# Kernel optimization log

Hardware: AMD Instinct MI355X
Metric: run time of the kernel (lower is better)

The kernel has to match this reference:

```python
import jax, jax.numpy as jnp
import numpy as np

SCORE_THR = 0.05
IOU_THR = 0.5
STD = np.array([0.1, 0.1, 0.2, 0.2], dtype=np.float32)


def _regress_and_clip(reg_pred, anchors, h, w):
    # reg_pred [B,4,A], anchors [A,4] (x1,y1,x2,y2) -> boxes [B,A,4]
    std = jnp.asarray(STD)
    widths = anchors[:, 2] - anchors[:, 0]
    heights = anchors[:, 3] - anchors[:, 1]
    cx = anchors[:, 0] + 0.5 * widths
    cy = anchors[:, 1] + 0.5 * heights
    reg = reg_pred * std[None, :, None]
    dx, dy, dw, dh = reg[:, 0], reg[:, 1], reg[:, 2], reg[:, 3]  # each [B,A]
    pred_cx = cx + dx * widths
    pred_cy = cy + dy * heights
    pred_w = jnp.exp(dw) * widths
    pred_h = jnp.exp(dh) * heights
    x1 = jnp.maximum(pred_cx - 0.5 * pred_w, 0.0)
    y1 = pred_cy - 0.5 * pred_h
    x2 = pred_cx + 0.5 * pred_w
    y2 = pred_cy + 0.5 * pred_h
    # clip_anchors
    x1 = jnp.maximum(x1, 0.0)
    y1 = jnp.maximum(y1, 0.0)
    x2 = jnp.minimum(x2, jnp.float32(w))
    y2 = jnp.minimum(y2, jnp.float32(h))
    return jnp.stack([x1, y1, x2, y2], axis=-1)  # [B,A,4] (= permuted boxes_pred)


def _iou_one_vs_all(box, boxes):
    ix1 = jnp.maximum(box[0], boxes[:, 0])
    iy1 = jnp.maximum(box[1], boxes[:, 1])
    ix2 = jnp.minimum(box[2], boxes[:, 2])
    iy2 = jnp.minimum(box[3], boxes[:, 3])
    inter = jnp.maximum(ix2 - ix1, 0.0) * jnp.maximum(iy2 - iy1, 0.0)
    a0 = (box[2] - box[0]) * (box[3] - box[1])
    a1 = (boxes[:, 2] - boxes[:, 0]) * (boxes[:, 3] - boxes[:, 1])
    return inter / jnp.maximum(a0 + a1 - inter, 1e-9)


def _nms_keep(boxes, scores):
    # Greedy NMS (torchvision semantics): returns bool keep mask over all anchors.
    valid = scores > SCORE_THR
    order = jnp.argsort(jnp.where(valid, -scores, jnp.inf))  # desc by score, invalid last
    b = boxes[order]
    keep0 = valid[order]
    n = boxes.shape[0]
    idx = jnp.arange(n)
    def body(i, keep):
        iou = _iou_one_vs_all(b[i], b)
        sup = keep[i] & (iou > IOU_THR) & (idx > i)
        return keep & (~sup)
    keep_sorted = jax.lax.fori_loop(0, n, body, keep0)
    return jnp.zeros(n, dtype=bool).at[order].set(keep_sorted)


def _keep_mask(boxes, cls_pred):
    # boxes [B,A,4], cls_pred [B,C,A] -> keep [B,C,A]
    per_class = jax.vmap(_nms_keep, in_axes=(None, 0))
    return jax.vmap(per_class, in_axes=(0, 0))(boxes, cls_pred)


def setup_inputs() -> dict:
    key = jax.random.key(0)
    k1, k2, k3, k4 = jax.random.split(key, 4)
    B, C, A, H, W = 2, 80, 1024, 2048, 2048
    image = jax.random.normal(k1, (B, 3, H, W), dtype=jnp.float32)
    cls_pred = jax.random.uniform(k2, (B, C, A), dtype=jnp.float32)  # sigmoid-like scores
    reg_pred = jax.random.normal(k3, (B, 4, A), dtype=jnp.float32)
    kc, ks = jax.random.split(k4)
    cxy = jax.random.uniform(kc, (A, 2), minval=0.0, maxval=float(W), dtype=jnp.float32)
    wh = jax.random.uniform(ks, (A, 2), minval=16.0, maxval=256.0, dtype=jnp.float32)
    anchors = jnp.concatenate([cxy - 0.5 * wh, cxy + 0.5 * wh], axis=1)  # [A,4] x1y1x2y2
    return {"image": image, "cls_pred": cls_pred, "reg_pred": reg_pred, "anchors": anchors}


def reference(image, cls_pred, reg_pred, anchors):
    B, _, H, W = image.shape
    boxes = _regress_and_clip(reg_pred, anchors, H, W)      # [B,A,4]
    keep = _keep_mask(boxes, cls_pred)                      # [B,C,A] bool
    scores_out = jnp.where(keep, cls_pred, 0.0)             # [B,C,A]
    boxes_out = jnp.where(keep[..., None], boxes[:, None, :, :], 0.0)  # [B,C,A,4]
    # Fixed-shape packing of the module's ragged [scores, cls, boxes] output:
    # per (batch, class, anchor): (score, x1, y1, x2, y2), zeros where suppressed.
    return jnp.concatenate([scores_out[..., None], boxes_out], axis=-1)  # [B,C,A,5]
```

## Files before the change

kernel.cpp:

```cpp
#include <hip/hip_runtime.h>
#include <stdint.h>

#define BATCH 2
#define NCLS 80
#define NP (BATCH * NCLS)
#define NA 1024
#define NWORD 16
#define NWBLK 64
#define IMG_W 2048.0f
#define IMG_H 2048.0f

__device__ __forceinline__ unsigned enc_f32(float f) {
  unsigned u = __float_as_uint(f);
  return (u & 0x80000000u) ? ~u : (u | 0x80000000u);
}

__device__ __forceinline__ unsigned long long shflx64(unsigned long long v, int m) {
  int lo = __shfl_xor((int)(unsigned)v, m, 64);
  int hi = __shfl_xor((int)(unsigned)(v >> 32), m, 64);
  return ((unsigned long long)(unsigned)hi << 32) | (unsigned)lo;
}

__device__ __forceinline__ void cas64(unsigned long long& x, unsigned long long& y, bool up) {
  if ((x > y) == up) { unsigned long long t = x; x = y; y = t; }
}

__global__ __launch_bounds__(256) void prep_kernel(
    const float* __restrict__ cls_pred,
    const float* __restrict__ reg_pred,
    const float* __restrict__ anchors,
    unsigned long long* __restrict__ skeyG,
    float4* __restrict__ sboxG,
    int* __restrict__ nvalidG,
    unsigned long long* __restrict__ W)
{
#pragma clang fp contract(off)
  const int tid = threadIdx.x;
  __shared__ __align__(16) unsigned char smem[24832];

  if (blockIdx.x < NP) {
    const int bc = blockIdx.x;
    const int b  = bc / NCLS;
    float4*             obox = (float4*)(smem);
    unsigned long long* skey = (unsigned long long*)(smem + 16384);
    int*                cntS = (int*)(smem + 24576);

    if (tid == 0) *cntS = 0;
    __syncthreads();

    const float* regb = reg_pred + (size_t)b * 4 * NA;
    const float* scb  = cls_pred + (size_t)bc * NA;

    float4 s4 = ((const float4*)scb)[tid];
    float4 x4 = ((const float4*)(regb + 0 * NA))[tid];
    float4 y4 = ((const float4*)(regb + 1 * NA))[tid];
    float4 w4 = ((const float4*)(regb + 2 * NA))[tid];
    float4 h4 = ((const float4*)(regb + 3 * NA))[tid];
    float ss[4]  = {s4.x, s4.y, s4.z, s4.w};
    float dxs[4] = {x4.x, x4.y, x4.z, x4.w};
    float dys[4] = {y4.x, y4.y, y4.z, y4.w};
    float dws[4] = {w4.x, w4.y, w4.z, w4.w};
    float dhs[4] = {h4.x, h4.y, h4.z, h4.w};

    unsigned long long r[4];
    int localcnt = 0;
#pragma unroll
    for (int m = 0; m < 4; ++m) {
      const int a = tid * 4 + m;
      float4 an = ((const float4*)anchors)[a];
      float w  = an.z - an.x;
      float h  = an.w - an.y;
      float cx = an.x + 0.5f * w;
      float cy = an.y + 0.5f * h;
      float dx = dxs[m] * 0.1f;
      float dy = dys[m] * 0.1f;
      float dw = dws[m] * 0.2f;
      float dh = dhs[m] * 0.2f;
      float pcx = cx + dx * w;
      float pcy = cy + dy * h;
      float pw  = expf(dw) * w;
      float ph  = expf(dh) * h;
      float x1 = fmaxf(pcx - 0.5f * pw, 0.0f);
      float y1 = pcy - 0.5f * ph;
      x1 = fmaxf(x1, 0.0f);
      y1 = fmaxf(y1, 0.0f);
      float x2 = fminf(pcx + 0.5f * pw, IMG_W);
      float y2 = fminf(pcy + 0.5f * ph, IMG_H);
      obox[a] = make_float4(x1, y1, x2, y2);

      float s    = ss[m];
      bool valid = (s > 0.05f);
      localcnt  += valid ? 1 : 0;
      float key  = valid ? -s : __int_as_float(0x7f800000);
      r[m] = ((unsigned long long)enc_f32(key) << 32) | (unsigned)a;
    }
    atomicAdd(cntS, localcnt);

#pragma unroll
    for (int kk = 1; kk <= 10; ++kk) {
      const int k = 1 << kk;
#pragma unroll
      for (int jj = kk - 1; jj >= 0; --jj) {
        const int j = 1 << jj;
        if (j >= 256) {
          __syncthreads();
#pragma unroll
          for (int m = 0; m < 4; ++m) skey[tid * 4 + m] = r[m];
          __syncthreads();
#pragma unroll
          for (int m = 0; m < 4; ++m) {
            const int e = tid * 4 + m;
            unsigned long long o = skey[e ^ j];
            const bool up = ((e & k) == 0);
            const bool lo = ((e & j) == 0);
            unsigned long long mn = (r[m] < o) ? r[m] : o;
            unsigned long long mx = (r[m] < o) ? o : r[m];
            r[m] = (lo == up) ? mn : mx;
          }
        } else if (j >= 4) {
          const int d = j >> 2;
          const bool lo = ((tid & d) == 0);
#pragma unroll
          for (int m = 0; m < 4; ++m) {
            const int e = tid * 4 + m;
            const bool up = ((e & k) == 0);
            unsigned long long o = shflx64(r[m], d);
            unsigned long long mn = (r[m] < o) ? r[m] : o;
            unsigned long long mx = (r[m] < o) ? o : r[m];
            r[m] = (lo == up) ? mn : mx;
          }
        } else if (j == 2) {
          const bool up = (((tid * 4) & k) == 0);
          cas64(r[0], r[2], up);
          cas64(r[1], r[3], up);
        } else {
          const bool up01 = (((tid * 4 + 0) & k) == 0);
          const bool up23 = (((tid * 4 + 2) & k) == 0);
          cas64(r[0], r[1], up01);
          cas64(r[2], r[3], up23);
        }
      }
    }

    unsigned long long* pk = skeyG + (size_t)bc * NA;
    float4* pb = sboxG + (size_t)bc * NA;
#pragma unroll
    for (int m = 0; m < 4; ++m) {
      unsigned long long kv = r[m];
      pk[tid * 4 + m] = kv;
      pb[tid * 4 + m] = obox[(int)(unsigned)kv];
    }
    if (tid == 0) nvalidG[bc] = *cntS;

  } else {
    const int wb   = blockIdx.x - NP;
    const int b    = wb >> 5;
    const int sub  = wb & 31;
    const int rblk = sub >> 1;
    const int qh   = sub & 1;
    const int lane = tid & 63;
    const int wq   = tid >> 6;

    float4* sb = (float4*)(smem);

    const float* regb = reg_pred + (size_t)b * 4 * NA;
    for (int a = tid; a < NA; a += 256) {
      float4 an = ((const float4*)anchors)[a];
      float w  = an.z - an.x;
      float h  = an.w - an.y;
      float cx = an.x + 0.5f * w;
      float cy = an.y + 0.5f * h;
      float dx = regb[0 * NA + a] * 0.1f;
      float dy = regb[1 * NA + a] * 0.1f;
      float dw = regb[2 * NA + a] * 0.2f;
      float dh = regb[3 * NA + a] * 0.2f;
      float pcx = cx + dx * w;
      float pcy = cy + dy * h;
      float pw  = expf(dw) * w;
      float ph  = expf(dh) * h;
      float x1 = fmaxf(pcx - 0.5f * pw, 0.0f);
      float y1 = pcy - 0.5f * ph;
      x1 = fmaxf(x1, 0.0f);
      y1 = fmaxf(y1, 0.0f);
      float x2 = fminf(pcx + 0.5f * pw, IMG_W);
      float y2 = fminf(pcy + 0.5f * ph, IMG_H);
      sb[a] = make_float4(x1, y1, x2, y2);
    }
    __syncthreads();

    const int r = rblk * 64 + lane;
    float4 br = sb[r];
    float  ar = (br.z - br.x) * (br.w - br.y);
    unsigned long long* wrow = W + ((size_t)b * NA + r) * NWORD;

#pragma unroll
    for (int k2 = 0; k2 < 2; ++k2) {
      const int kw = qh * 8 + wq * 2 + k2;
      const int jbase = kw * 64;
      unsigned long long bits = 0ull;
#pragma unroll 8
      for (int jj = 0; jj < 64; ++jj) {
        float4 bj = sb[jbase + jj];
        float  aj = (bj.z - bj.x) * (bj.w - bj.y);
        float ix1 = fmaxf(br.x, bj.x);
        float iy1 = fmaxf(br.y, bj.y);
        float ix2 = fminf(br.z, bj.z);
        float iy2 = fminf(br.w, bj.w);
        float inter = fmaxf(ix2 - ix1, 0.0f) * fmaxf(iy2 - iy1, 0.0f);
        float un = fmaxf((ar + aj) - inter, 1e-9f);
        bool sup = ((inter + inter) - un) > un * 5.9604644775390625e-8f;
        bits |= sup ? (1ull << jj) : 0ull;
      }
      wrow[kw] = bits;
    }
  }
}

__global__ __launch_bounds__(128) void scan_kernel(
    const unsigned long long* __restrict__ skeyG,
    const float4* __restrict__ sboxG,
    const unsigned long long* __restrict__ W,
    const int* __restrict__ nvalidG,
    float* __restrict__ out)
{
  const int p    = blockIdx.x;
  const int b    = p / NCLS;
  const int tid  = threadIdx.x;
  const int lane = tid & 63;
  const int wid  = tid >> 6;

  __shared__ unsigned long long rowsL[2][64 * 17];
  __shared__ unsigned long long diagL[2][64];
  __shared__ int oL[NA];
  __shared__ unsigned long long KorigL[NWORD];
  __shared__ unsigned long long keptS[NWORD];
  __shared__ __align__(16) float outAll[NA * 5];

  if (tid < NWORD) { KorigL[tid] = 0ull; keptS[tid] = 0ull; }

  const int nv = nvalidG[p];
  const int nchunk = (nv + 63) >> 6;
  const unsigned long long* pk = skeyG + (size_t)p * NA;
  const unsigned long long* Wb = W + (size_t)b * NA * NWORD;

#pragma unroll
  for (int t = 0; t < 8; ++t) {
    int r = t * 128 + tid;
    oL[r] = (int)(unsigned)pk[r];
  }
  __syncthreads();

  const int rsub = lane >> 4;
  const int wsub = lane & 15;

  if (wid == 1 && nchunk > 0) {
    unsigned long long pre[16];
#pragma unroll
    for (int t = 0; t < 16; ++t) {
      int orow = oL[t * 4 + rsub];
      pre[t] = Wb[(size_t)orow * NWORD + wsub];
    }
#pragma unroll
    for (int t = 0; t < 16; ++t)
      rowsL[0][(t * 4 + rsub) * 17 + wsub] = pre[t];
    int om = oL[lane];
    int wsel = om >> 6, bsel = om & 63;
    unsigned long long d = 0ull;
#pragma unroll 16
    for (int si = 0; si < 64; ++si)
      d |= ((rowsL[0][si * 17 + wsel] >> bsel) & 1ull) << si;
    diagL[0][lane] = d;
  }
  __syncthreads();

  for (int c = 0; c < nchunk; ++c) {
    const int cbuf = c & 1;
    if (wid == 1) {
      if (c + 1 < nchunk) {
        const int nbuf = cbuf ^ 1;
        unsigned long long pre[16];
#pragma unroll
        for (int t = 0; t < 16; ++t) {
          int orow = oL[(c + 1) * 64 + t * 4 + rsub];
          pre[t] = Wb[(size_t)orow * NWORD + wsub];
        }
#pragma unroll
        for (int t = 0; t < 16; ++t)
          rowsL[nbuf][(t * 4 + rsub) * 17 + wsub] = pre[t];
        int om = oL[(c + 1) * 64 + lane];
        int wsel = om >> 6, bsel = om & 63;
        unsigned long long d = 0ull;
#pragma unroll 16
        for (int si = 0; si < 64; ++si)
          d |= ((rowsL[nbuf][si * 17 + wsel] >> bsel) & 1ull) << si;
        diagL[nbuf][lane] = d;
      }
    } else {
      const int sMine = c * 64 + lane;
      const int oMine = oL[sMine];

      unsigned long long pp = 0ull;
      if (c) {
#pragma unroll
        for (int k = 0; k < NWORD; ++k)
          pp |= rowsL[cbuf][lane * 17 + k] & KorigL[k];
      }

      unsigned long long diag = diagL[cbuf][lane] & ((1ull << lane) - 1ull);

      unsigned long long valid = __ballot(sMine < nv);
      unsigned long long S     = __ballot(pp != 0ull);
      unsigned long long K  = 0ull;
      unsigned long long Dd = (~valid) | S;
      for (int round = 0; round < 64; ++round) {
        unsigned long long und = ~Dd;
        if (und == 0ull) break;
        bool me_und  = (und >> lane) & 1ull;
        bool blocked = (diag & (K | und)) != 0ull;
        bool isSupp  = (diag & K) != 0ull;
        unsigned long long kb  = __ballot(me_und && !blocked);
        unsigned long long sbm = __ballot(me_und && isSupp);
        K  |= kb;
        Dd |= kb | sbm;
      }
      if (lane == 0) keptS[c] = K;

      if ((K >> lane) & 1ull)
        atomicOr(&KorigL[oMine >> 6], 1ull << (oMine & 63));
    }
    __syncthreads();
  }

  const float4* pb = sboxG + (size_t)p * NA;
#pragma unroll
  for (int t = 0; t < 8; ++t) {
    int r = t * 128 + tid;
    unsigned long long kv = pk[r];
    float4 bx = pb[r];
    int orig = (int)(unsigned)kv;
    bool kp = (keptS[r >> 6] >> (r & 63)) & 1ull;
    float sc = 0.0f;
    float4 ob = make_float4(0.0f, 0.0f, 0.0f, 0.0f);
    if (kp) {
      sc = -__uint_as_float(~(unsigned)(kv >> 32));
      ob = bx;
    }
    float* oa = outAll + (size_t)orig * 5;
    oa[0] = sc; oa[1] = ob.x; oa[2] = ob.y; oa[3] = ob.z; oa[4] = ob.w;
  }
  __syncthreads();

  float4* og = (float4*)(out + (size_t)p * NA * 5);
  const float4* ol = (const float4*)outAll;
  for (int t4 = tid; t4 < (NA * 5) / 4; t4 += 128) og[t4] = ol[t4];
}

__global__ __launch_bounds__(256) void nms_mono_kernel(
    const float* __restrict__ cls_pred,
    const float* __restrict__ reg_pred,
    const float* __restrict__ anchors,
    float* __restrict__ out)
{
#pragma clang fp contract(off)
  const int bc  = blockIdx.x;
  const int b   = bc / NCLS;
  const int tid = threadIdx.x;
  const int BNT = 256, BPT = 4;

  __shared__ __align__(16) unsigned char smem[49152];
  float4*             obox  = (float4*)(smem);
  float4*             sbox  = (float4*)(smem + 16384);
  unsigned long long* skey  = (unsigned long long*)(smem + 32768);
  float*              sarea = (float*)(smem + 40960);
  int*                keepL = (int*)(smem + 45056);

  const float* regb = reg_pred + (size_t)b * 4 * NA;
  const float* scb  = cls_pred + (size_t)bc * NA;
  for (int a = tid; a < NA; a += BNT) {
    float4 an = ((const float4*)anchors)[a];
    float w  = an.z - an.x;
    float h  = an.w - an.y;
    float cx = an.x + 0.5f * w;
    float cy = an.y + 0.5f * h;
    float dx = regb[0 * NA + a] * 0.1f;
    float dy = regb[1 * NA + a] * 0.1f;
    float dw = regb[2 * NA + a] * 0.2f;
    float dh = regb[3 * NA + a] * 0.2f;
    float pcx = cx + dx * w;
    float pcy = cy + dy * h;
    float pw  = expf(dw) * w;
    float ph  = expf(dh) * h;
    float x1 = fmaxf(fmaxf(pcx - 0.5f * pw, 0.0f), 0.0f);
    float y1 = fmaxf(pcy - 0.5f * ph, 0.0f);
    float x2 = fminf(pcx + 0.5f * pw, IMG_W);
    float y2 = fminf(pcy + 0.5f * ph, IMG_H);
    obox[a] = make_float4(x1, y1, x2, y2);
    float s   = scb[a];
    float key = (s > 0.05f) ? -s : __int_as_float(0x7f800000);
    skey[a] = ((unsigned long long)enc_f32(key) << 32) | (unsigned)a;
  }
  __syncthreads();
  for (int k = 2; k <= NA; k <<= 1) {
    for (int j = k >> 1; j > 0; j >>= 1) {
      for (int m = tid; m < NA; m += BNT) {
        int mx = m ^ j;
        if (mx > m) {
          unsigned long long va = skey[m];
          unsigned long long vb = skey[mx];
          bool up = ((m & k) == 0);
          if ((va > vb) == up) { skey[m] = vb; skey[mx] = va; }
        }
      }
      __syncthreads();
    }
  }
  float4 bj[4]; float aj[4]; int kj[4];
#pragma unroll
  for (int m = 0; m < BPT; ++m) {
    int r = tid + m * BNT;
    unsigned long long kv = skey[r];
    int orig = (int)(unsigned)kv;
    float4 bx = obox[orig];
    sbox[r] = bx;
    float ar = (bx.z - bx.x) * (bx.w - bx.y);
    sarea[r] = ar;
    int kp = ((unsigned)(kv >> 32) != 0xFF800000u) ? 1 : 0;
    keepL[r] = kp;
    bj[m] = bx; aj[m] = ar; kj[m] = kp;
  }
  for (int i = 0; i < NA; ++i) {
    __syncthreads();
    if (keepL[i] == 0) continue;
    float4 bi = sbox[i];
    float  ai = sarea[i];
#pragma unroll
    for (int m = 0; m < BPT; ++m) {
      int j = tid + m * BNT;
      if (j > i && kj[m]) {
        float ix1 = fmaxf(bi.x, bj[m].x);
        float iy1 = fmaxf(bi.y, bj[m].y);
        float ix2 = fminf(bi.z, bj[m].z);
        float iy2 = fminf(bi.w, bj[m].w);
        float inter = fmaxf(ix2 - ix1, 0.0f) * fmaxf(iy2 - iy1, 0.0f);
        float un = fmaxf(ai + aj[m] - inter, 1e-9f);
        if (inter / un > 0.5f) { kj[m] = 0; keepL[j] = 0; }
      }
    }
  }
  __syncthreads();
  float4* outbox = obox;
  float*  outsc  = sarea;
#pragma unroll
  for (int m = 0; m < BPT; ++m) {
    int r = tid + m * BNT;
    unsigned long long kv = skey[r];
    int orig = (int)(unsigned)kv;
    float  sc = 0.0f;
    float4 bx = make_float4(0.0f, 0.0f, 0.0f, 0.0f);
    if (kj[m]) {
      sc = -__uint_as_float(~(unsigned)(kv >> 32));
      bx = sbox[r];
    }
    outsc[orig]  = sc;
    outbox[orig] = bx;
  }
  __syncthreads();
  float* ob = out + (size_t)bc * NA * 5;
  for (int a = tid; a < NA; a += BNT) {
    float4 bx = outbox[a];
    float* o = ob + (size_t)a * 5;
    o[0] = outsc[a]; o[1] = bx.x; o[2] = bx.y; o[3] = bx.z; o[4] = bx.w;
  }
}

extern "C" void kernel_launch(void* const* d_in, const int* in_sizes, int n_in,
                              void* d_out, int out_size, void* d_ws, size_t ws_size,
                              hipStream_t stream) {
  const float* cls = (const float*)d_in[1];
  const float* reg = (const float*)d_in[2];
  const float* anc = (const float*)d_in[3];
  float* out = (float*)d_out;

  const size_t off_key = 0;
  const size_t off_box = off_key + (size_t)NP * NA * 8;
  const size_t off_w   = off_box + (size_t)NP * NA * 16;
  const size_t off_nv  = off_w + (size_t)BATCH * NA * NWORD * 8;
  const size_t need    = off_nv + (size_t)NP * sizeof(int);

  if (ws_size < need) {
    nms_mono_kernel<<<dim3(NP), dim3(256), 0, stream>>>(cls, reg, anc, out);
    return;
  }

  char* ws = (char*)d_ws;
  unsigned long long* skeyG = (unsigned long long*)(ws + off_key);
  float4*             sboxG = (float4*)(ws + off_box);
  unsigned long long* Wm    = (unsigned long long*)(ws + off_w);
  int*                nvG   = (int*)(ws + off_nv);

  prep_kernel<<<dim3(NP + NWBLK), dim3(256), 0, stream>>>(
      cls, reg, anc, skeyG, sboxG, nvG, Wm);
  scan_kernel<<<dim3(NP), dim3(128), 0, stream>>>(skeyG, sboxG, Wm, nvG, out);
}
```

Baseline: 164.5 us.

## Fuse prep and scan into one cooperative kernel with grid sync

Replaces the two-kernel prep/scan pipeline with a single cooperative kernel. Per-class sorted keys, boxes and valid counts stay in shared memory across a grid-wide sync instead of going through global workspace, and only the IoU bitmask matrix is written to global memory. The scan phase uses one wave to prefetch the next chunk's mask rows and diagonal while another wave resolves the current chunk. Output rows are staged in shared memory and written with coalesced float4 stores. This removes a kernel launch boundary and the workspace round-trip, but it relies on cooperative launch support, and the grid sync plus heavy shared-memory use could limit residency.

```diff
diff --git a/kernel.cpp b/kernel.cpp
--- a/kernel.cpp
+++ b/kernel.cpp
@@ -1,5 +1,8 @@
 #include <hip/hip_runtime.h>
+#include <hip/hip_cooperative_groups.h>
 #include <stdint.h>
+
+namespace cg = cooperative_groups;
 
 #define BATCH 2
 #define NCLS 80
@@ -23,6 +26,314 @@
 
 __device__ __forceinline__ void cas64(unsigned long long& x, unsigned long long& y, bool up) {
   if ((x > y) == up) { unsigned long long t = x; x = y; y = t; }
+}
+
+__global__ __launch_bounds__(256) void fused_kernel(
+    const float* __restrict__ cls_pred,
+    const float* __restrict__ reg_pred,
+    const float* __restrict__ anchors,
+    unsigned long long* __restrict__ W,
+    float* __restrict__ out)
+{
+#pragma clang fp contract(off)
+  const int tid = threadIdx.x;
+
+  __shared__ __align__(16) unsigned char smem[47616];
+  float4*             obox  = (float4*)(smem);
+  unsigned long long* skey  = (unsigned long long*)(smem + 16384);
+  int*                cntS  = (int*)(smem + 24576);
+  int*                oL    = (int*)(smem + 24832);
+  unsigned long long* rowsL = (unsigned long long*)(smem + 28928);
+  unsigned long long* diagL = (unsigned long long*)(smem + 46336);
+  unsigned long long* KorigL= (unsigned long long*)(smem + 47360);
+  unsigned long long* keptS = (unsigned long long*)(smem + 47488);
+  float*              outAll= (float*)(smem + 24832);
+
+  unsigned long long r[4] = {0ull, 0ull, 0ull, 0ull};
+
+  if (blockIdx.x < NP) {
+    const int bc = blockIdx.x;
+    const int b  = bc / NCLS;
+
+    if (tid == 0) *cntS = 0;
+    __syncthreads();
+
+    const float* regb = reg_pred + (size_t)b * 4 * NA;
+    const float* scb  = cls_pred + (size_t)bc * NA;
+
+    float4 s4 = ((const float4*)scb)[tid];
+    float4 x4 = ((const float4*)(regb + 0 * NA))[tid];
+    float4 y4 = ((const float4*)(regb + 1 * NA))[tid];
+    float4 w4 = ((const float4*)(regb + 2 * NA))[tid];
+    float4 h4 = ((const float4*)(regb + 3 * NA))[tid];
+    float ss[4]  = {s4.x, s4.y, s4.z, s4.w};
+    float dxs[4] = {x4.x, x4.y, x4.z, x4.w};
+    float dys[4] = {y4.x, y4.y, y4.z, y4.w};
+    float dws[4] = {w4.x, w4.y, w4.z, w4.w};
+    float dhs[4] = {h4.x, h4.y, h4.z, h4.w};
+
+    int localcnt = 0;
+#pragma unroll
+    for (int m = 0; m < 4; ++m) {
+      const int a = tid * 4 + m;
+      float4 an = ((const float4*)anchors)[a];
+      float w  = an.z - an.x;
+      float h  = an.w - an.y;
+      float cx = an.x + 0.5f * w;
+      float cy = an.y + 0.5f * h;
+      float dx = dxs[m] * 0.1f;
+      float dy = dys[m] * 0.1f;
+      float dw = dws[m] * 0.2f;
+      float dh = dhs[m] * 0.2f;
+      float pcx = cx + dx * w;
+      float pcy = cy + dy * h;
+      float pw  = expf(dw) * w;
+      float ph  = expf(dh) * h;
+      float x1 = fmaxf(pcx - 0.5f * pw, 0.0f);
+      float y1 = pcy - 0.5f * ph;
+      x1 = fmaxf(x1, 0.0f);
+      y1 = fmaxf(y1, 0.0f);
+      float x2 = fminf(pcx + 0.5f * pw, IMG_W);
+      float y2 = fminf(pcy + 0.5f * ph, IMG_H);
+      obox[a] = make_float4(x1, y1, x2, y2);
+
+      float s    = ss[m];
+      bool valid = (s > 0.05f);
+      localcnt  += valid ? 1 : 0;
+      float key  = valid ? -s : __int_as_float(0x7f800000);
+      r[m] = ((unsigned long long)enc_f32(key) << 32) | (unsigned)a;
+    }
+    atomicAdd(cntS, localcnt);
+
+#pragma unroll
+    for (int kk = 1; kk <= 10; ++kk) {
+      const int k = 1 << kk;
+#pragma unroll
+      for (int jj = kk - 1; jj >= 0; --jj) {
+        const int j = 1 << jj;
+        if (j >= 256) {
+          __syncthreads();
+#pragma unroll
+          for (int m = 0; m < 4; ++m) skey[tid * 4 + m] = r[m];
+          __syncthreads();
+#pragma unroll
+          for (int m = 0; m < 4; ++m) {
+            const int e = tid * 4 + m;
+            unsigned long long o = skey[e ^ j];
+            const bool up = ((e & k) == 0);
+            const bool lo = ((e & j) == 0);
+            unsigned long long mn = (r[m] < o) ? r[m] : o;
+            unsigned long long mx = (r[m] < o) ? o : r[m];
+            r[m] = (lo == up) ? mn : mx;
+          }
+        } else if (j >= 4) {
+          const int d = j >> 2;
+          const bool lo = ((tid & d) == 0);
+#pragma unroll
+          for (int m = 0; m < 4; ++m) {
+            const int e = tid * 4 + m;
+            const bool up = ((e & k) == 0);
+            unsigned long long o = shflx64(r[m], d);
+            unsigned long long mn = (r[m] < o) ? r[m] : o;
+            unsigned long long mx = (r[m] < o) ? o : r[m];
+            r[m] = (lo == up) ? mn : mx;
+          }
+        } else if (j == 2) {
+          const bool up = (((tid * 4) & k) == 0);
+          cas64(r[0], r[2], up);
+          cas64(r[1], r[3], up);
+        } else {
+          const bool up01 = (((tid * 4 + 0) & k) == 0);
+          const bool up23 = (((tid * 4 + 2) & k) == 0);
+          cas64(r[0], r[1], up01);
+          cas64(r[2], r[3], up23);
+        }
+      }
+    }
+
+  } else {
+    const int wb   = blockIdx.x - NP;
+    const int b    = wb >> 5;
+    const int sub  = wb & 31;
+    const int rblk = sub >> 1;
+    const int qh   = sub & 1;
+    const int lane = tid & 63;
+    const int wq   = tid >> 6;
+
+    float4* sb = obox;
+
+    const float* regb = reg_pred + (size_t)b * 4 * NA;
+    for (int a = tid; a < NA; a += 256) {
+      float4 an = ((const float4*)anchors)[a];
+      float w  = an.z - an.x;
+      float h  = an.w - an.y;
+      float cx = an.x + 0.5f * w;
+      float cy = an.y + 0.5f * h;
+      float dx = regb[0 * NA + a] * 0.1f;
+      float dy = regb[1 * NA + a] * 0.1f;
+      float dw = regb[2 * NA + a] * 0.2f;
+      float dh = regb[3 * NA + a] * 0.2f;
+      float pcx = cx + dx * w;
+      float pcy = cy + dy * h;
+      float pw  = expf(dw) * w;
+      float ph  = expf(dh) * h;
+      float x1 = fmaxf(pcx - 0.5f * pw, 0.0f);
+      float y1 = pcy - 0.5f * ph;
+      x1 = fmaxf(x1, 0.0f);
+      y1 = fmaxf(y1, 0.0f);
+      float x2 = fminf(pcx + 0.5f * pw, IMG_W);
+      float y2 = fminf(pcy + 0.5f * ph, IMG_H);
+      sb[a] = make_float4(x1, y1, x2, y2);
+    }
+    __syncthreads();
+
+    const int rr = rblk * 64 + lane;
+    float4 br = sb[rr];
+    float  ar = (br.z - br.x) * (br.w - br.y);
+    unsigned long long* wrow = W + ((size_t)b * NA + rr) * NWORD;
+
+#pragma unroll
+    for (int k2 = 0; k2 < 2; ++k2) {
+      const int kw = qh * 8 + wq * 2 + k2;
+      const int jbase = kw * 64;
+      unsigned long long bits = 0ull;
+#pragma unroll 8
+      for (int jj = 0; jj < 64; ++jj) {
+        float4 bj = sb[jbase + jj];
+        float  aj = (bj.z - bj.x) * (bj.w - bj.y);
+        float ix1 = fmaxf(br.x, bj.x);
+        float iy1 = fmaxf(br.y, bj.y);
+        float ix2 = fminf(br.z, bj.z);
+        float iy2 = fminf(br.w, bj.w);
+        float inter = fmaxf(ix2 - ix1, 0.0f) * fmaxf(iy2 - iy1, 0.0f);
+        float un = fmaxf((ar + aj) - inter, 1e-9f);
+        bool sup = ((inter + inter) - un) > un * 5.9604644775390625e-8f;
+        bits |= sup ? (1ull << jj) : 0ull;
+      }
+      wrow[kw] = bits;
+    }
+  }
+
+  __threadfence();
+  cg::this_grid().sync();
+
+  if (blockIdx.x >= NP) return;
+
+  const int p    = blockIdx.x;
+  const int b    = p / NCLS;
+  const int lane = tid & 63;
+  const int wid  = tid >> 6;
+
+#pragma unroll
+  for (int m = 0; m < 4; ++m) oL[tid * 4 + m] = (int)(unsigned)r[m];
+  if (tid < NWORD) { KorigL[tid] = 0ull; keptS[tid] = 0ull; }
+  __syncthreads();
+
+  const int nv = *cntS;
+  const int nchunk = (nv + 63) >> 6;
+  const unsigned long long* Wb = W + (size_t)b * NA * NWORD;
+
+  const int rsub = lane >> 4;
+  const int wsub = lane & 15;
+
+  if (wid == 1 && nchunk > 0) {
+    unsigned long long pre[16];
+#pragma unroll
+    for (int t = 0; t < 16; ++t) {
+      int orow = oL[t * 4 + rsub];
+      pre[t] = Wb[(size_t)orow * NWORD + wsub];
+    }
+#pragma unroll
+    for (int t = 0; t < 16; ++t)
+      rowsL[(t * 4 + rsub) * 17 + wsub] = pre[t];
+    int om = oL[lane];
+    int wsel = om >> 6, bsel = om & 63;
+    unsigned long long d = 0ull;
+#pragma unroll 16
+    for (int si = 0; si < 64; ++si)
+      d |= ((rowsL[si * 17 + wsel] >> bsel) & 1ull) << si;
+    diagL[lane] = d;
+  }
+  __syncthreads();
+
+  for (int c = 0; c < nchunk; ++c) {
+    const int cbuf = c & 1;
+    if (wid == 1) {
+      if (c + 1 < nchunk) {
+        const int nbuf = cbuf ^ 1;
+        unsigned long long pre[16];
+#pragma unroll
+        for (int t = 0; t < 16; ++t) {
+          int orow = oL[(c + 1) * 64 + t * 4 + rsub];
+          pre[t] = Wb[(size_t)orow * NWORD + wsub];
+        }
+#pragma unroll
+        for (int t = 0; t < 16; ++t)
+          rowsL[nbuf * 1088 + (t * 4 + rsub) * 17 + wsub] = pre[t];
+        int om = oL[(c + 1) * 64 + lane];
+        int wsel = om >> 6, bsel = om & 63;
+        unsigned long long d = 0ull;
+#pragma unroll 16
+        for (int si = 0; si < 64; ++si)
+          d |= ((rowsL[nbuf * 1088 + si * 17 + wsel] >> bsel) & 1ull) << si;
+        diagL[nbuf * 64 + lane] = d;
+      }
+    } else if (wid == 0) {
+      const int sMine = c * 64 + lane;
+      const int oMine = oL[sMine];
+
+      unsigned long long pp = 0ull;
+      if (c) {
+#pragma unroll
+        for (int k = 0; k < NWORD; ++k)
+          pp |= rowsL[cbuf * 1088 + lane * 17 + k] & KorigL[k];
+      }
+
+      unsigned long long diag = diagL[cbuf * 64 + lane] & ((1ull << lane) - 1ull);
+
+      unsigned long long valid = __ballot(sMine < nv);
+      unsigned long long S     = __ballot(pp != 0ull);
+      unsigned long long K  = 0ull;
+      unsigned long long Dd = (~valid) | S;
+      for (int round = 0; round < 64; ++round) {
+        unsigned long long und = ~Dd;
+        if (und == 0ull) break;
+        bool me_und  = (und >> lane) & 1ull;
+        bool blocked = (diag & (K | und)) != 0ull;
+        bool isSupp  = (diag & K) != 0ull;
+        unsigned long long kb  = __ballot(me_und && !blocked);
+        unsigned long long sbm = __ballot(me_und && isSupp);
+        K  |= kb;
+        Dd |= kb | sbm;
+      }
+      if (lane == 0) keptS[c] = K;
+
+      if ((K >> lane) & 1ull)
+        atomicOr(&KorigL[oMine >> 6], 1ull << (oMine & 63));
+    }
+    __syncthreads();
+  }
+
+#pragma unroll
+  for (int m = 0; m < 4; ++m) {
+    const int e = tid * 4 + m;
+    unsigned long long kv = r[m];
+    int orig = (int)(unsigned)kv;
+    bool kp = (keptS[e >> 6] >> (e & 63)) & 1ull;
+    float sc = 0.0f;
+    float4 ob = make_float4(0.0f, 0.0f, 0.0f, 0.0f);
+    if (kp) {
+      sc = -__uint_as_float(~(unsigned)(kv >> 32));
+      ob = obox[orig];
+    }
+    float* oa = outAll + (size_t)orig * 5;
+    oa[0] = sc; oa[1] = ob.x; oa[2] = ob.y; oa[3] = ob.z; oa[4] = ob.w;
+  }
+  __syncthreads();
+
+  float4* og = (float4*)(out + (size_t)p * NA * 5);
+  const float4* ol = (const float4*)outAll;
+  for (int t4 = tid; t4 < (NA * 5) / 4; t4 += 256) og[t4] = ol[t4];
 }
 
 __global__ __launch_bounds__(256) void prep_kernel(
@@ -486,11 +797,7 @@
   const size_t off_w   = off_box + (size_t)NP * NA * 16;
   const size_t off_nv  = off_w + (size_t)BATCH * NA * NWORD * 8;
   const size_t need    = off_nv + (size_t)NP * sizeof(int);
-
-  if (ws_size < need) {
-    nms_mono_kernel<<<dim3(NP), dim3(256), 0, stream>>>(cls, reg, anc, out);
-    return;
-  }
+  const size_t needW   = off_nv;
 
   char* ws = (char*)d_ws;
   unsigned long long* skeyG = (unsigned long long*)(ws + off_key);
@@ -498,6 +805,33 @@
   unsigned long long* Wm    = (unsigned long long*)(ws + off_w);
   int*                nvG   = (int*)(ws + off_nv);
 
+  static int coop_ok = -1;
+  if (coop_ok < 0) {
+    int dev = 0, v = 0;
+    if (hipGetDevice(&dev) == hipSuccess)
+      hipDeviceGetAttribute(&v, hipDeviceAttributeCooperativeLaunch, dev);
+    coop_ok = v ? 1 : 0;
+  }
+
+  if (coop_ok && ws_size >= needW) {
+    void* ka[5];
+    ka[0] = (void*)&cls;
+    ka[1] = (void*)&reg;
+    ka[2] = (void*)&anc;
+    ka[3] = (void*)&Wm;
+    ka[4] = (void*)&out;
+    hipError_t e = hipLaunchCooperativeKernel(
+        (const void*)fused_kernel, dim3(NP + NWBLK), dim3(256), ka, 0, stream);
+    if (e == hipSuccess) return;
+    (void)hipGetLastError();
+    coop_ok = 0;
+  }
+
+  if (ws_size < need) {
+    nms_mono_kernel<<<dim3(NP), dim3(256), 0, stream>>>(cls, reg, anc, out);
+    return;
+  }
+
   prep_kernel<<<dim3(NP + NWBLK), dim3(256), 0, stream>>>(
       cls, reg, anc, skeyG, sboxG, nvG, Wm);
   scan_kernel<<<dim3(NP), dim3(128), 0, stream>>>(skeyG, sboxG, Wm, nvG, out);
```

Result: slower. 224.6 us (+36.5%).

## Widen scan kernel to four waves with a three-stage row/diagonal pipeline

Applied to the files above, without the earlier changes.

The scan kernel goes from 128 to 256 threads. Row gathering (wave 1) now runs two chunks ahead into a triple buffer. Diagonal-bit extraction moves to two dedicated waves, each handling 32 rows, and runs one chunk ahead. The serial scan wave then only ORs the two diagonal halves, taking gather and transpose work off the critical path per chunk, at the cost of more shared memory and a larger block.

```diff
diff --git a/kernel.cpp b/kernel.cpp
--- a/kernel.cpp
+++ b/kernel.cpp
@@ -216,7 +216,7 @@
   }
 }
 
-__global__ __launch_bounds__(128) void scan_kernel(
+__global__ __launch_bounds__(256) void scan_kernel(
     const unsigned long long* __restrict__ skeyG,
     const float4* __restrict__ sboxG,
     const unsigned long long* __restrict__ W,
@@ -229,8 +229,9 @@
   const int lane = tid & 63;
   const int wid  = tid >> 6;
 
-  __shared__ unsigned long long rowsL[2][64 * 17];
-  __shared__ unsigned long long diagL[2][64];
+  __shared__ unsigned long long rowsL[3][64 * 17];
+  __shared__ unsigned long long diagLo[2][64];
+  __shared__ unsigned long long diagHi[2][64];
   __shared__ int oL[NA];
   __shared__ unsigned long long KorigL[NWORD];
   __shared__ unsigned long long keptS[NWORD];
@@ -244,58 +245,81 @@
   const unsigned long long* Wb = W + (size_t)b * NA * NWORD;
 
 #pragma unroll
-  for (int t = 0; t < 8; ++t) {
-    int r = t * 128 + tid;
+  for (int t = 0; t < 4; ++t) {
+    int r = t * 256 + tid;
     oL[r] = (int)(unsigned)pk[r];
   }
   __syncthreads();
 
-  const int rsub = lane >> 4;
-  const int wsub = lane & 15;
-
-  if (wid == 1 && nchunk > 0) {
-    unsigned long long pre[16];
-#pragma unroll
-    for (int t = 0; t < 16; ++t) {
-      int orow = oL[t * 4 + rsub];
-      pre[t] = Wb[(size_t)orow * NWORD + wsub];
-    }
-#pragma unroll
-    for (int t = 0; t < 16; ++t)
-      rowsL[0][(t * 4 + rsub) * 17 + wsub] = pre[t];
+  if (nchunk > 0) {
+    const int half = wid >> 1;
+    const int slot = tid & 127;
+    const int rsub8 = slot >> 4;
+    const int wsub  = slot & 15;
+    if (half == 0 || nchunk > 1) {
+      const int cbase = half * 64;
+      unsigned long long pre[8];
+#pragma unroll
+      for (int t = 0; t < 8; ++t) {
+        int orow = oL[cbase + t * 8 + rsub8];
+        pre[t] = Wb[(size_t)orow * NWORD + wsub];
+      }
+#pragma unroll
+      for (int t = 0; t < 8; ++t)
+        rowsL[half][(t * 8 + rsub8) * 17 + wsub] = pre[t];
+    }
+  }
+  __syncthreads();
+
+  if (nchunk > 0 && wid >= 2) {
+    const int sbase = (wid - 2) * 32;
     int om = oL[lane];
     int wsel = om >> 6, bsel = om & 63;
     unsigned long long d = 0ull;
 #pragma unroll 16
-    for (int si = 0; si < 64; ++si)
+    for (int s = 0; s < 32; ++s) {
+      int si = sbase + s;
       d |= ((rowsL[0][si * 17 + wsel] >> bsel) & 1ull) << si;
-    diagL[0][lane] = d;
-  }
-  __syncthreads();
+    }
+    if (wid == 2) diagLo[0][lane] = d; else diagHi[0][lane] = d;
+  }
+  __syncthreads();
+
+  const int rsub = lane >> 4;
+  const int wsub = lane & 15;
 
   for (int c = 0; c < nchunk; ++c) {
-    const int cbuf = c & 1;
     if (wid == 1) {
-      if (c + 1 < nchunk) {
-        const int nbuf = cbuf ^ 1;
+      if (c + 2 < nchunk) {
+        const int nb = (c + 2) % 3;
         unsigned long long pre[16];
 #pragma unroll
         for (int t = 0; t < 16; ++t) {
-          int orow = oL[(c + 1) * 64 + t * 4 + rsub];
+          int orow = oL[(c + 2) * 64 + t * 4 + rsub];
           pre[t] = Wb[(size_t)orow * NWORD + wsub];
         }
 #pragma unroll
         for (int t = 0; t < 16; ++t)
-          rowsL[nbuf][(t * 4 + rsub) * 17 + wsub] = pre[t];
+          rowsL[nb][(t * 4 + rsub) * 17 + wsub] = pre[t];
+      }
+    } else if (wid >= 2) {
+      if (c + 1 < nchunk) {
+        const int nb = (c + 1) % 3;
+        const int par = (c + 1) & 1;
+        const int sbase = (wid - 2) * 32;
         int om = oL[(c + 1) * 64 + lane];
         int wsel = om >> 6, bsel = om & 63;
         unsigned long long d = 0ull;
 #pragma unroll 16
-        for (int si = 0; si < 64; ++si)
-          d |= ((rowsL[nbuf][si * 17 + wsel] >> bsel) & 1ull) << si;
-        diagL[nbuf][lane] = d;
+        for (int s = 0; s < 32; ++s) {
+          int si = sbase + s;
+          d |= ((rowsL[nb][si * 17 + wsel] >> bsel) & 1ull) << si;
+        }
+        if (wid == 2) diagLo[par][lane] = d; else diagHi[par][lane] = d;
       }
     } else {
+      const int cb  = c % 3;
+      const int par = c & 1;
       const int sMine = c * 64 + lane;
       const int oMine = oL[sMine];
 
@@ -303,10 +327,11 @@
       if (c) {
 #pragma unroll
         for (int k = 0; k < NWORD; ++k)
-          pp |= rowsL[cbuf][lane * 17 + k] & KorigL[k];
-      }
-
-      unsigned long long diag = diagL[cbuf][lane] & ((1ull << lane) - 1ull);
+          pp |= rowsL[cb][lane * 17 + k] & KorigL[k];
+      }
+
+      unsigned long long diag =
+          (diagLo[par][lane] | diagHi[par][lane]) & ((1ull << lane) - 1ull);
 
       unsigned long long valid = __ballot(sMine < nv);
       unsigned long long S     = __ballot(pp != 0ull);
@@ -333,8 +358,8 @@
 
   const float4* pb = sboxG + (size_t)p * NA;
 #pragma unroll
-  for (int t = 0; t < 8; ++t) {
-    int r = t * 128 + tid;
+  for (int t = 0; t < 4; ++t) {
+    int r = t * 256 + tid;
     unsigned long long kv = pk[r];
     float4 bx = pb[r];
     int orig = (int)(unsigned)kv;
@@ -352,7 +377,7 @@
 
   float4* og = (float4*)(out + (size_t)p * NA * 5);
   const float4* ol = (const float4*)outAll;
-  for (int t4 = tid; t4 < (NA * 5) / 4; t4 += 128) og[t4] = ol[t4];
+  for (int t4 = tid; t4 < (NA * 5) / 4; t4 += 256) og[t4] = ol[t4];
 }
 
 __global__ __launch_bounds__(256) void nms_mono_kernel(
@@ -466,6 +491,7 @@
   }
   __syncthreads();
   float* ob = out + (size_t)bc * NA * 5;
+  for (int a = tid; a < BNT * BPT; a += BNT) {}
   for (int a = tid; a < NA; a += BNT) {
     float4 bx = outbox[a];
     float* o = ob + (size_t)a * 5;
@@ -500,5 +526,5 @@
 
   prep_kernel<<<dim3(NP + NWBLK), dim3(256), 0, stream>>>(
       cls, reg, anc, skeyG, sboxG, nvG, Wm);
-  scan_kernel<<<dim3(NP), dim3(128), 0, stream>>>(skeyG, sboxG, Wm, nvG, out);
-}
+  scan_kernel<<<dim3(NP), dim3(256), 0, stream>>>(skeyG, sboxG, Wm, nvG, out);
+}
```

New measurement: 153.9 us. -6.4%, faster.
